# Performance work log

Measured on AMD Instinct MI355X. Metric: run time of the kernel, lower is better.

The kernel has to match this reference:

```python
import jax, jax.numpy as jnp
import numpy as np
import math

# Model dims
B, S, D, H = 2, 2048, 1024, 16
DH = D // H  # 64
TAU = 0.2
EPS = 1e-5

# Unit-scaling scale factors (constraint = gmean of fwd/bwd scales)
# Linear: gmean(fan_in**-0.5, fan_out**-0.5) = (fan_in*fan_out)**-0.25
# Matmul (m,k)@(k,n): gmean(k**-0.5, n**-0.5, m**-0.5) = (m*k*n)**(-1/6)
# Softmax over dim n: gmean(n/1.31, n/1.65) (empirical constants from unit_scaling)
# GELU: gmean(1/0.588, 1/0.675)
MM_SCALE = (S * S * DH) ** (-1.0 / 6.0)
SM_SCALE = S / math.sqrt(1.31 * 1.65)
GELU_SCALE = (0.588 * 0.675) ** -0.5
SQRT_TAU = math.sqrt(TAU)
SQRT_1MTAU = math.sqrt(1.0 - TAU)


def u_linear(x, w, b=None):
    fan_out, fan_in = w.shape
    scale = (fan_in * fan_out) ** -0.25
    y = x @ w.T
    if b is not None:
        y = y + b
    return y * scale


def layer_norm(x, w, b):
    m = jnp.mean(x, axis=-1, keepdims=True)
    v = jnp.mean(jnp.square(x - m), axis=-1, keepdims=True)
    return (x - m) * jax.lax.rsqrt(v + EPS) * w + b


def setup_inputs() -> dict:
    key = jax.random.key(0)
    ks = jax.random.split(key, 8)
    return {
        "x": jax.random.normal(ks[0], (B, S, D), jnp.float32),
        "w_qkv": jax.random.normal(ks[1], (3 * D, D), jnp.float32),
        "w_o": jax.random.normal(ks[2], (D, D), jnp.float32),
        "w1": jax.random.normal(ks[3], (4 * D, D), jnp.float32),
        "b1": jnp.zeros((4 * D,), jnp.float32),
        "w2": jax.random.normal(ks[4], (D, 4 * D), jnp.float32),
        "b2": jnp.zeros((D,), jnp.float32),
        "ln1_w": jnp.ones((D,), jnp.float32),
        "ln1_b": jnp.zeros((D,), jnp.float32),
        "ln2_w": jnp.ones((D,), jnp.float32),
        "ln2_b": jnp.zeros((D,), jnp.float32),
    }


def reference(x, w_qkv, w_o, w1, b1, w2, b2, ln1_w, ln1_b, ln2_w, ln2_b):
    # --- MHSA branch (residual_split forward is identity; tau enters at add) ---
    skip = x
    h = layer_norm(x, ln1_w, ln1_b)
    qkv = u_linear(h, w_qkv)  # [B,S,3D]
    # einops 'b s (d z h) -> z b h s d' with z=3, h=H
    qkv = qkv.reshape(B, S, DH, 3, H)
    q = jnp.transpose(qkv[:, :, :, 0, :], (0, 3, 1, 2))  # [B,H,S,DH]
    k = jnp.transpose(qkv[:, :, :, 1, :], (0, 3, 1, 2))
    v = jnp.transpose(qkv[:, :, :, 2, :], (0, 3, 1, 2))
    scores = jnp.einsum("bhsd,bhtd->bhst", q, k) * MM_SCALE
    attn = jax.nn.softmax(scores, axis=-1) * SM_SCALE
    # dropout: eval mode -> identity
    av = jnp.einsum("bhst,bhtd->bhsd", attn, v) * MM_SCALE
    av = jnp.transpose(av, (0, 2, 1, 3)).reshape(B, S, D)  # b h s d -> b s (h d)
    attn_out = u_linear(av, w_o)
    x = SQRT_TAU * attn_out + SQRT_1MTAU * skip  # residual_add

    # --- MLP branch ---
    skip = x
    h = layer_norm(x, ln2_w, ln2_b)
    h = u_linear(h, w1, b1)
    h = jax.nn.gelu(h, approximate=False) * GELU_SCALE
    h = u_linear(h, w2, b2)
    return SQRT_TAU * h + SQRT_1MTAU * skip
```

## Files before the change

kernel.cpp:

```cpp
#include <hip/hip_runtime.h>
#include <hip/hip_bf16.h>
#include <math.h>

typedef __hip_bfloat16 bf16;
typedef __attribute__((ext_vector_type(8))) short short8;
typedef __attribute__((ext_vector_type(4))) float floatx4;

#define B_   2
#define S_   2048
#define D_   1024
#define H_   16
#define DH_  64
#define BS_  4096
#define D3_  3072
#define DF_  4096

__device__ __forceinline__ float tof(float v) { return v; }
__device__ __forceinline__ float tof(bf16 v) { return __bfloat162float(v); }

__device__ __forceinline__ void gload_lds16(const bf16* g, bf16* l) {
  __builtin_amdgcn_global_load_lds(
      (const __attribute__((address_space(1))) unsigned int*)g,
      (__attribute__((address_space(3))) unsigned int*)l, 16, 0, 0);
}

#define VMCNT(n) asm volatile("s_waitcnt vmcnt(" #n ")" ::: "memory")

__global__ __launch_bounds__(256) void cvt_f32_bf16(
    const float* __restrict__ in, bf16* __restrict__ out, int n4) {
  int i = blockIdx.x * 256 + threadIdx.x;
  if (i >= n4) return;
  float4 v = ((const float4*)in)[i];
  bf16 o[4] = {__float2bfloat16(v.x), __float2bfloat16(v.y),
               __float2bfloat16(v.z), __float2bfloat16(v.w)};
  ((ulong1*)out)[i] = *(ulong1*)o;
}

__global__ __launch_bounds__(256) void cvt_all(
    const float* __restrict__ wqkv, const float* __restrict__ wo,
    const float* __restrict__ w1, bf16* __restrict__ wqb,
    bf16* __restrict__ wob, bf16* __restrict__ w1b) {
  const int g = blockIdx.x * 256 + threadIdx.x;
  if (g < 786432) {
    const int n2 = g >> 8;
    const int col = (g & 255) * 4;
    const int z = n2 >> 10, hh = (n2 >> 6) & 15, d = n2 & 63;
    const int n = d * 48 + z * 16 + hh;
    float4 v = *(const float4*)(wqkv + (size_t)n * 1024 + col);
    bf16 o[4] = {__float2bfloat16(v.x), __float2bfloat16(v.y),
                 __float2bfloat16(v.z), __float2bfloat16(v.w)};
    *(unsigned long long*)(wqb + (size_t)n2 * 1024 + col) =
        *(unsigned long long*)o;
  } else if (g < 1048576) {
    const int g2 = g - 786432;
    float4 v = ((const float4*)wo)[g2];
    bf16 o[4] = {__float2bfloat16(v.x), __float2bfloat16(v.y),
                 __float2bfloat16(v.z), __float2bfloat16(v.w)};
    ((unsigned long long*)wob)[g2] = *(unsigned long long*)o;
  } else {
    const int g2 = g - 1048576;
    float4 v = ((const float4*)w1)[g2];
    bf16 o[4] = {__float2bfloat16(v.x), __float2bfloat16(v.y),
                 __float2bfloat16(v.z), __float2bfloat16(v.w)};
    ((unsigned long long*)w1b)[g2] = *(unsigned long long*)o;
  }
}

template <bool FUSE, bool INIT, typename TA, typename TS>
__global__ __launch_bounds__(256) void resid_ln_kernel(
    const TA* __restrict__ a, const TA* __restrict__ a2,
    const TS* __restrict__ skip,
    const float* __restrict__ w, const float* __restrict__ bias,
    bf16* __restrict__ hout, float st, float s1t,
    float* __restrict__ oinit, const float* __restrict__ b2,
    float cb, float cs) {
  const int row = blockIdx.x;
  const int tid = threadIdx.x;
  const int base = tid * 4;
  const size_t roff = (size_t)row * D_;

  float xv[4];
#pragma unroll
  for (int i = 0; i < 4; i++) {
    float v = tof(a[roff + base + i]);
    if (FUSE) v = st * (v + tof(a2[roff + base + i]))
                  + s1t * tof(skip[roff + base + i]);
    xv[i] = v;
  }
  if (INIT) {
#pragma unroll
    for (int i = 0; i < 4; i++)
      oinit[roff + base + i] = cs * xv[i] + cb * b2[base + i];
  }

  float ls = 0.f, lq = 0.f;
#pragma unroll
  for (int i = 0; i < 4; i++) { ls += xv[i]; lq += xv[i] * xv[i]; }

  __shared__ float ssum[256];
  __shared__ float ssq[256];
  ssum[tid] = ls; ssq[tid] = lq;
  __syncthreads();
  for (int off = 128; off > 0; off >>= 1) {
    if (tid < off) { ssum[tid] += ssum[tid + off]; ssq[tid] += ssq[tid + off]; }
    __syncthreads();
  }
  const float mean = ssum[0] * (1.0f / D_);
  const float var  = ssq[0] * (1.0f / D_) - mean * mean;
  const float rstd = rsqrtf(var + 1e-5f);

#pragma unroll
  for (int i = 0; i < 4; i++) {
    float v = (xv[i] - mean) * rstd * w[base + i] + bias[base + i];
    hout[roff + base + i] = __float2bfloat16(v);
  }
}

__global__ __launch_bounds__(256) void reduce_ffn2(
    const bf16* __restrict__ p0, const bf16* __restrict__ p1,
    float* __restrict__ out, float sc) {
  const size_t i = ((size_t)blockIdx.x * 256 + threadIdx.x) * 8;
  short8 a = *(const short8*)(p0 + i);
  short8 b = *(const short8*)(p1 + i);
  bf16 t0[8], t1[8];
  *(short8*)t0 = a; *(short8*)t1 = b;
  float4 o0 = *(float4*)(out + i);
  float4 o1 = *(float4*)(out + i + 4);
#pragma unroll
  for (int e = 0; e < 4; e++) {
    ((float*)&o0)[e] += sc * (__bfloat162float(t0[e]) + __bfloat162float(t1[e]));
    ((float*)&o1)[e] += sc * (__bfloat162float(t0[e + 4]) + __bfloat162float(t1[e + 4]));
  }
  *(float4*)(out + i) = o0;
  *(float4*)(out + i + 4) = o1;
}

__global__ __launch_bounds__(256) void combine_attn(
    const bf16* __restrict__ O0, const bf16* __restrict__ O1,
    const float* __restrict__ l0, const float* __restrict__ l1,
    bf16* __restrict__ att, float sc) {
  const size_t i = ((size_t)blockIdx.x * 256 + threadIdx.x) * 8;
  const int srow = (int)(i >> 10);
  const int h = (int)(i >> 6) & 15;
  const float inv = sc / (l0[srow * H_ + h] + l1[srow * H_ + h]);
  short8 a = *(const short8*)(O0 + i);
  short8 b = *(const short8*)(O1 + i);
  bf16 t0[8], t1[8], o[8];
  *(short8*)t0 = a; *(short8*)t1 = b;
#pragma unroll
  for (int e = 0; e < 8; e++)
    o[e] = __float2bfloat16((tof(t0[e]) + tof(t1[e])) * inv);
  *(short8*)(att + i) = *(short8*)o;
}

template <int EPI, typename TC>
__global__ __launch_bounds__(512, 2) void gemm_mfma256(
    const bf16* __restrict__ A, const bf16* __restrict__ Bw,
    TC* __restrict__ C, int M, int N, int K, float scale,
    const float* __restrict__ bias, float st) {
  __shared__ __align__(16) bf16 As[2][2][128][64];
  __shared__ __align__(16) bf16 Bs[2][2][128][64];

  const int tid = threadIdx.x;
  const int lane = tid & 63;
  const int w = tid >> 6;
  const int wm = w >> 2;
  const int wn = w & 3;
  const int quad = lane >> 4;
  const int l16 = lane & 15;

  const int nbx = N >> 8;
  const int nwg = nbx * (M >> 8);
  int bid = blockIdx.x;
  bid = (bid & 7) * (nwg >> 3) + (bid >> 3);
  const size_t bm = (size_t)(bid / nbx) * 256;
  const size_t bn = (size_t)(bid % nbx) * 256;

  const bf16* gsrc[4][2];
  bf16* ldsp[4][2];
#pragma unroll
  for (int i = 0; i < 2; i++) {
    const int G = tid + i * 512;
    const int cr = G >> 3;
    const int gs8 = ((G & 7) ^ (cr & 7)) * 8;
    const int ra = ((cr >> 6) << 7) + (cr & 63);
    const int rb = ((cr >> 5) << 6) + (cr & 31);
    gsrc[0][i] = A  + (bm + ra) * (size_t)K + gs8;
    gsrc[2][i] = A  + (bm + ra + 64) * (size_t)K + gs8;
    gsrc[1][i] = Bw + (bn + rb) * (size_t)K + gs8;
    gsrc[3][i] = Bw + (bn + rb + 32) * (size_t)K + gs8;
    ldsp[0][i] = &As[0][0][0][0] + G * 8;
    ldsp[2][i] = &As[0][1][0][0] + G * 8;
    ldsp[1][i] = &Bs[0][0][0][0] + G * 8;
    ldsp[3][i] = &Bs[0][1][0][0] + G * 8;
  }

  auto STAGE = [&](int c, int tn) {
    const int boff = (tn & 1) * 16384;
    gload_lds16(gsrc[c][0] + (size_t)tn * 64, ldsp[c][0] + boff);
    gload_lds16(gsrc[c][1] + (size_t)tn * 64, ldsp[c][1] + boff);
  };

  const int ksw0 = (quad ^ (l16 & 7)) * 8;
  const int ksw1 = ((4 + quad) ^ (l16 & 7)) * 8;

  floatx4 acc[8][4];
#pragma unroll
  for (int i = 0; i < 8; i++)
#pragma unroll
    for (int j = 0; j < 4; j++) acc[i][j] = {0.f, 0.f, 0.f, 0.f};

  short8 af[4][2], bv[2][2];

  auto READ_A = [&](int b, int h) {
#pragma unroll
    for (int mf = 0; mf < 4; mf++) {
      const bf16* p = &As[b][h][wm * 64 + mf * 16 + l16][0];
      af[mf][0] = *(const short8*)(p + ksw0);
      af[mf][1] = *(const short8*)(p + ksw1);
    }
  };
  auto READ_B = [&](int b, int bh) {
#pragma unroll
    for (int nf = 0; nf < 2; nf++) {
      const bf16* p = &Bs[b][bh][wn * 32 + nf * 16 + l16][0];
      bv[nf][0] = *(const short8*)(p + ksw0);
      bv[nf][1] = *(const short8*)(p + ksw1);
    }
  };
  auto MFMA16 = [&](int mb, int nb) {
#pragma unroll
    for (int mf = 0; mf < 4; mf++)
#pragma unroll
      for (int nf = 0; nf < 2; nf++) {
        floatx4 c = acc[mb + mf][nb + nf];
        c = __builtin_amdgcn_mfma_f32_16x16x32_bf16(af[mf][0], bv[nf][0], c, 0, 0, 0);
        c = __builtin_amdgcn_mfma_f32_16x16x32_bf16(af[mf][1], bv[nf][1], c, 0, 0, 0);
        acc[mb + mf][nb + nf] = c;
      }
  };

  STAGE(0, 0); STAGE(1, 0); STAGE(2, 0); STAGE(3, 0);
  VMCNT(4);
  __builtin_amdgcn_s_barrier();
  __builtin_amdgcn_sched_barrier(0);

  const int NT = K >> 6;
#pragma unroll 1
  for (int t = 0; t < NT; t++) {
    const int b = t & 1;
    const bool nl = (t + 1 < NT);
    READ_A(b, 0);
    READ_B(b, 0);
    if (nl) STAGE(0, t + 1);
    __builtin_amdgcn_s_barrier();
    __builtin_amdgcn_sched_barrier(0);
    __builtin_amdgcn_s_setprio(1);
    MFMA16(0, 0);
    __builtin_amdgcn_s_setprio(0);
    if (nl) { VMCNT(2); } else { VMCNT(0); }
    __builtin_amdgcn_s_barrier();
    __builtin_amdgcn_sched_barrier(0);
    READ_B(b, 1);
    if (nl) STAGE(1, t + 1);
    __builtin_amdgcn_s_barrier();
    __builtin_amdgcn_sched_barrier(0);
    __builtin_amdgcn_s_setprio(1);
    MFMA16(0, 2);
    __builtin_amdgcn_s_setprio(0);
    __builtin_amdgcn_s_barrier();
    __builtin_amdgcn_sched_barrier(0);
    READ_A(b, 1);
    if (nl) STAGE(2, t + 1);
    __builtin_amdgcn_s_barrier();
    __builtin_amdgcn_sched_barrier(0);
    __builtin_amdgcn_s_setprio(1);
    MFMA16(4, 2);
    __builtin_amdgcn_s_setprio(0);
    __builtin_amdgcn_s_barrier();
    __builtin_amdgcn_sched_barrier(0);
    READ_B(b, 0);
    if (nl) STAGE(3, t + 1);
    __builtin_amdgcn_s_barrier();
    __builtin_amdgcn_sched_barrier(0);
    __builtin_amdgcn_s_setprio(1);
    MFMA16(4, 0);
    __builtin_amdgcn_s_setprio(0);
    if (nl) { VMCNT(4); } else { VMCNT(0); }
    __builtin_amdgcn_s_barrier();
    __builtin_amdgcn_sched_barrier(0);
  }

  float sc_eff = scale;
  if (EPI == 2) sc_eff = (bn < 1024) ? st : scale;
  float bias4[4];
  if (EPI == 1) {
#pragma unroll
    for (int j = 0; j < 4; j++) bias4[j] = bias[bn + wn * 64 + j * 16 + l16];
  }
#pragma unroll
  for (int mi = 0; mi < 8; mi++) {
    const size_t r0 = bm + wm * 128 + (mi >> 2) * 64 + (mi & 3) * 16 + quad * 4;
#pragma unroll
    for (int r = 0; r < 4; r++) {
      const size_t rowoff = (r0 + r) * (size_t)N + bn + wn * 64 + l16;
#pragma unroll
      for (int j = 0; j < 4; j++) {
        float v = acc[mi][j][r];
        if (EPI == 2) {
          ((bf16*)C)[rowoff + j * 16] = __float2bfloat16(v * sc_eff);
        } else {
          float u = (v + bias4[j]) * scale;
          float tt = u * (0.7978845608f + 0.0356774081f * u * u);
          float e = __builtin_amdgcn_exp2f(tt * 2.8853900818f);
          float th = 1.0f - 2.0f * __builtin_amdgcn_rcpf(e + 1.0f);
          ((bf16*)C)[rowoff + j * 16] =
              __float2bfloat16(0.5f * u * (1.0f + th) * st);
        }
      }
    }
  }
}

__global__ __launch_bounds__(512, 2) void gemm_mfma128(
    const bf16* __restrict__ A, const bf16* __restrict__ Bw,
    bf16* __restrict__ C, bf16* __restrict__ C2, int M, int N, int K) {
  __shared__ __align__(16) bf16 As[2][2][128][64];
  __shared__ __align__(16) bf16 Bs[2][2][64][64];

  const int tid = threadIdx.x;
  const int lane = tid & 63;
  const int w = tid >> 6;
  const int wm = w >> 2;
  const int wn = w & 3;
  const int quad = lane >> 4;
  const int l16 = lane & 15;

  const int nbx = N >> 7;
  const int nwg = nbx * (M >> 8) * 2;
  int bid = blockIdx.x;
  bid = (bid & 7) * (nwg >> 3) + (bid >> 3);
  const int split = bid & 1;
  const int tile = bid >> 1;
  const size_t bm = (size_t)(tile / nbx) * 256;
  const size_t bn = (size_t)(tile % nbx) * 128;
  const int lda = K * 2;
  const int koff = split * K;

  const bf16* gA[2][2];
  bf16* lA[2][2];
#pragma unroll
  for (int i = 0; i < 2; i++) {
    const int G = tid + i * 512;
    const int cr = G >> 3;
    const int gs8 = ((G & 7) ^ (cr & 7)) * 8;
    const int ra = ((cr >> 6) << 7) + (cr & 63);
    gA[0][i] = A + (bm + ra) * (size_t)lda + koff + gs8;
    gA[1][i] = A + (bm + ra + 64) * (size_t)lda + koff + gs8;
    lA[0][i] = &As[0][0][0][0] + G * 8;
    lA[1][i] = &As[0][1][0][0] + G * 8;
  }
  const bf16* gB[2];
  bf16* lB[2];
  {
    const int cr = tid >> 3;
    const int gs8 = ((tid & 7) ^ (cr & 7)) * 8;
    gB[0] = Bw + (bn + cr) * (size_t)lda + koff + gs8;
    gB[1] = Bw + (bn + 64 + cr) * (size_t)lda + koff + gs8;
    lB[0] = &Bs[0][0][0][0] + tid * 8;
    lB[1] = &Bs[0][1][0][0] + tid * 8;
  }

  auto STAGE_A = [&](int h, int tn) {
    const int boff = (tn & 1) * 16384;
    gload_lds16(gA[h][0] + (size_t)tn * 64, lA[h][0] + boff);
    gload_lds16(gA[h][1] + (size_t)tn * 64, lA[h][1] + boff);
  };
  auto STAGE_B = [&](int bh, int tn) {
    const int boff = (tn & 1) * 8192;
    gload_lds16(gB[bh] + (size_t)tn * 64, lB[bh] + boff);
  };

  const int ksw0 = (quad ^ (l16 & 7)) * 8;
  const int ksw1 = ((4 + quad) ^ (l16 & 7)) * 8;

  floatx4 acc[8][2];
#pragma unroll
  for (int i = 0; i < 8; i++)
#pragma unroll
    for (int j = 0; j < 2; j++) acc[i][j] = {0.f, 0.f, 0.f, 0.f};

  short8 af[4][2], bv[2][2];

  auto READ_A = [&](int b, int h) {
#pragma unroll
    for (int mf = 0; mf < 4; mf++) {
      const bf16* p = &As[b][h][wm * 64 + mf * 16 + l16][0];
      af[mf][0] = *(const short8*)(p + ksw0);
      af[mf][1] = *(const short8*)(p + ksw1);
    }
  };
  auto READ_BNF = [&](int b, int nf) {
    const bf16* p = &Bs[b][wn >> 1][(wn & 1) * 32 + nf * 16 + l16][0];
    bv[nf][0] = *(const short8*)(p + ksw0);
    bv[nf][1] = *(const short8*)(p + ksw1);
  };
  auto MFMA8 = [&](int mb, int nf) {
#pragma unroll
    for (int mf = 0; mf < 4; mf++) {
      floatx4 c = acc[mb + mf][nf];
      c = __builtin_amdgcn_mfma_f32_16x16x32_bf16(af[mf][0], bv[nf][0], c, 0, 0, 0);
      c = __builtin_amdgcn_mfma_f32_16x16x32_bf16(af[mf][1], bv[nf][1], c, 0, 0, 0);
      acc[mb + mf][nf] = c;
    }
  };

  STAGE_A(0, 0); STAGE_B(0, 0); STAGE_B(1, 0); STAGE_A(1, 0);
  VMCNT(2);
  __builtin_amdgcn_s_barrier();
  __builtin_amdgcn_sched_barrier(0);

  const int NT = K >> 6;
#pragma unroll 1
  for (int t = 0; t < NT; t++) {
    const int b = t & 1;
    const bool nl = (t + 1 < NT);
    READ_A(b, 0);
    READ_BNF(b, 0);
    if (nl) STAGE_A(0, t + 1);
    __builtin_amdgcn_s_barrier();
    __builtin_amdgcn_sched_barrier(0);
    __builtin_amdgcn_s_setprio(1);
    MFMA8(0, 0);
    __builtin_amdgcn_s_setprio(0);
    __builtin_amdgcn_s_barrier();
    __builtin_amdgcn_sched_barrier(0);
    READ_BNF(b, 1);
    if (nl) STAGE_B(0, t + 1);
    __builtin_amdgcn_s_barrier();
    __builtin_amdgcn_sched_barrier(0);
    __builtin_amdgcn_s_setprio(1);
    MFMA8(0, 1);
    __builtin_amdgcn_s_setprio(0);
    if (nl) { VMCNT(3); } else { VMCNT(0); }
    __builtin_amdgcn_s_barrier();
    __builtin_amdgcn_sched_barrier(0);
    READ_A(b, 1);
    if (nl) STAGE_B(1, t + 1);
    __builtin_amdgcn_s_barrier();
    __builtin_amdgcn_sched_barrier(0);
    __builtin_amdgcn_s_setprio(1);
    MFMA8(4, 1);
    __builtin_amdgcn_s_setprio(0);
    __builtin_amdgcn_s_barrier();
    __builtin_amdgcn_sched_barrier(0);
    if (nl) STAGE_A(1, t + 1);
    __builtin_amdgcn_s_barrier();
    __builtin_amdgcn_sched_barrier(0);
    __builtin_amdgcn_s_setprio(1);
    MFMA8(4, 0);
    __builtin_amdgcn_s_setprio(0);
    if (nl) { VMCNT(2); } else { VMCNT(0); }
    __builtin_amdgcn_s_barrier();
    __builtin_amdgcn_sched_barrier(0);
  }

  bf16* dst = split ? C2 : C;
#pragma unroll
  for (int mi = 0; mi < 8; mi++) {
    const size_t r0 = bm + wm * 128 + (mi >> 2) * 64 + (mi & 3) * 16 + quad * 4;
#pragma unroll
    for (int r = 0; r < 4; r++) {
      const size_t rowoff = (r0 + r) * (size_t)N + bn + wn * 32 + l16;
#pragma unroll
      for (int j = 0; j < 2; j++)
        dst[rowoff + j * 16] = __float2bfloat16(acc[mi][j][r]);
    }
  }
}

__global__ __launch_bounds__(512) void flash_attn_mfma(
    const bf16* __restrict__ qkv, bf16* __restrict__ O0,
    bf16* __restrict__ O1, float* __restrict__ lb0,
    float* __restrict__ lb1) {
  const int flat = (blockIdx.z * H_ + blockIdx.y) * 32 + blockIdx.x;
  const int g8 = flat & 7, slot = flat >> 3;
  const int hf = g8 * 4 + (slot >> 5);
  const int rem = slot & 31;
  const int qb = (rem >> 1) * 128;
  const int half = rem & 1;
  const int h = hf & 15, b = hf >> 4;

  const int tid = threadIdx.x;
  const int lane = tid & 63;
  const int wv = tid >> 6;
  const int quad = lane >> 4;
  const int l16 = lane & 15;

  __shared__ __align__(16) bf16 Ks[64][64];
  __shared__ __align__(16) bf16 Vt[2][64][64];
  __shared__ __align__(16) bf16 Ps[128][64];

  const bf16* Qb_ = qkv + (size_t)b * S_ * D3_ + h * DH_;
  const bf16* Kb_ = Qb_ + 1024 + (size_t)half * 1024 * D3_;
  const bf16* Vb_ = Qb_ + 2048 + (size_t)half * 1024 * D3_;

  short8 bq0, bq1;
  {
    const bf16* qrow = Qb_ + (size_t)(qb + wv * 16 + l16) * D3_ + quad * 8;
    bq0 = *(const short8*)(qrow);
    bq1 = *(const short8*)(qrow + 32);
  }

  float l_part = 0.f;
  floatx4 o[4];
#pragma unroll
  for (int fd = 0; fd < 4; fd++) o[fd] = {0.f, 0.f, 0.f, 0.f};

  const int prow = wv * 16 + l16;
  const int psw = (prow & 7) << 4;
  char* pbase = (char*)&Ps[0][0] + prow * 128;

  const bf16* ksrc =
      Kb_ + (size_t)(tid >> 3) * D3_ + (((tid & 7) ^ ((tid >> 3) & 7)) * 8);
  bf16* kdst = &Ks[0][0] + tid * 8;
  const int vj = tid & 63, vd = (tid >> 6) * 8;
  const int vjg = vj >> 3, vjr = vj & 7;

  const int ksw0 = (quad ^ (l16 & 7)) * 8;
  const int ksw1 = ((4 + quad) ^ (l16 & 7)) * 8;

  gload_lds16(ksrc, kdst);
  uint4 vreg = *(const uint4*)(Vb_ + (size_t)vj * D3_ + vd);

  const int NT = 1024 / 64;
#pragma unroll 1
  for (int t = 0; t < NT; t++) {
    const int cur = t & 1;
    {
      bf16 tmp[8];
      *(uint4*)tmp = vreg;
#pragma unroll
      for (int e = 0; e < 8; e++)
        Vt[cur][vd + e][((vjg ^ e) << 3) | vjr] = tmp[e];
    }
    __syncthreads();

    float st[4][4];
    __builtin_amdgcn_s_setprio(1);
#pragma unroll
    for (int fk = 0; fk < 4; fk++) {
      const bf16* kp = &Ks[fk * 16 + l16][0];
      short8 ak0 = *(const short8*)(kp + ksw0);
      short8 ak1 = *(const short8*)(kp + ksw1);
      floatx4 acc = {0.f, 0.f, 0.f, 0.f};
      acc = __builtin_amdgcn_mfma_f32_16x16x32_bf16(ak0, bq0, acc, 0, 0, 0);
      acc = __builtin_amdgcn_mfma_f32_16x16x32_bf16(ak1, bq1, acc, 0, 0, 0);
#pragma unroll
      for (int r = 0; r < 4; r++) st[fk][r] = acc[r];
    }
    __builtin_amdgcn_s_setprio(0);
    __syncthreads();

    if (t + 1 < NT) {
      gload_lds16(ksrc + (size_t)(t + 1) * 64 * D3_, kdst);
      vreg = *(const uint4*)(Vb_ + (size_t)((t + 1) * 64 + vj) * D3_ + vd);
    }

#pragma unroll
    for (int fk = 0; fk < 2; fk++) {
      bf16 pk[4];
#pragma unroll
      for (int r = 0; r < 4; r++) {
        const float p = __builtin_amdgcn_exp2f(st[fk][r]);
        l_part += p;
        pk[r] = __float2bfloat16(p);
      }
      *(uint2*)(pbase + ((fk * 32 + quad * 8) ^ psw)) = *(uint2*)pk;
    }
    short8 ap0 = *(const short8*)(pbase + ((quad * 16) ^ psw));
#pragma unroll
    for (int fk = 2; fk < 4; fk++) {
      bf16 pk[4];
#pragma unroll
      for (int r = 0; r < 4; r++) {
        const float p = __builtin_amdgcn_exp2f(st[fk][r]);
        l_part += p;
        pk[r] = __float2bfloat16(p);
      }
      *(uint2*)(pbase + ((fk * 32 + quad * 8) ^ psw)) = *(uint2*)pk;
    }
    short8 ap1 = *(const short8*)(pbase + ((64 + quad * 16) ^ psw));

    __builtin_amdgcn_s_setprio(1);
#pragma unroll
    for (int fd = 0; fd < 4; fd++) {
      const bf16* vp = &Vt[cur][fd * 16 + l16][0];
      short8 bv0 = *(const short8*)(vp + ksw0);
      short8 bv1 = *(const short8*)(vp + ksw1);
      o[fd] = __builtin_amdgcn_mfma_f32_16x16x32_bf16(ap0, bv0, o[fd], 0, 0, 0);
      o[fd] = __builtin_amdgcn_mfma_f32_16x16x32_bf16(ap1, bv1, o[fd], 0, 0, 0);
    }
    __builtin_amdgcn_s_setprio(0);
  }

  l_part += __shfl_xor(l_part, 16);
  l_part += __shfl_xor(l_part, 32);

  bf16* Oo = half ? O1 : O0;
  float* lo = half ? lb1 : lb0;
  if (quad == 0)
    lo[(size_t)(b * S_ + qb + wv * 16 + l16) * H_ + h] = l_part;
#pragma unroll
  for (int r = 0; r < 4; r++) {
    const size_t base =
        ((size_t)(b * S_ + qb + wv * 16 + quad * 4 + r)) * D_ + h * DH_;
#pragma unroll
    for (int fd = 0; fd < 4; fd++)
      Oo[base + fd * 16 + l16] = __float2bfloat16(o[fd][r]);
  }
}

extern "C" void kernel_launch(void* const* d_in, const int* in_sizes, int n_in,
                              void* d_out, int out_size, void* d_ws, size_t ws_size,
                              hipStream_t stream) {
  const float* x     = (const float*)d_in[0];
  const float* w_qkv = (const float*)d_in[1];
  const float* w_o   = (const float*)d_in[2];
  const float* w1    = (const float*)d_in[3];
  const float* b1    = (const float*)d_in[4];
  const float* w2    = (const float*)d_in[5];
  const float* b2    = (const float*)d_in[6];
  const float* ln1w  = (const float*)d_in[7];
  const float* ln1b  = (const float*)d_in[8];
  const float* ln2w  = (const float*)d_in[9];
  const float* ln2b  = (const float*)d_in[10];
  float* out = (float*)d_out;
  bf16* ws  = (bf16*)d_ws;

  bf16* h1   = ws;
  bf16* wqb  = ws + 4194304;
  bf16* wob  = ws + 7340032;
  bf16* qkv  = ws + 8388608;
  bf16* w1b  = ws + 25165824;
  bf16* Ob0  = ws + 20971520;
  bf16* Ob1  = ws;
  float* l0f = (float*)(ws + 4194304);
  float* l1f = l0f + 65536;
  bf16* att  = Ob0;
  bf16* w2b  = ws;
  bf16* Po   = ws + 8388608;
  bf16* h2   = ws + 4194304;
  bf16* g    = ws + 8388608;
  bf16* Pf0  = ws + 4194304;
  bf16* Pf1  = ws + 25165824;

  const float MM_SCALE   = (float)pow((double)S_ * S_ * DH_, -1.0 / 6.0);
  const float SM_SCALE   = (float)((double)S_ / sqrt(1.31 * 1.65));
  const float GELU_SCALE = (float)pow(0.588 * 0.675, -0.5);
  const float SQRT_TAU   = (float)sqrt(0.2);
  const float SQRT_1MT   = (float)sqrt(0.8);
  const float LOG2E      = 1.4426950408889634f;
  const float qkv_scale  = (float)pow((double)D_ * D3_, -0.25);
  const float o_scale    = (float)pow((double)D_ * D_, -0.25);
  const float w1_scale   = (float)pow((double)D_ * DF_, -0.25);
  const float w2_scale   = (float)pow((double)DF_ * D_, -0.25);

  cvt_all<<<8192, 256, 0, stream>>>(w_qkv, w_o, w1, wqb, wob, w1b);
  resid_ln_kernel<false, false, float, float><<<BS_, 256, 0, stream>>>(
      x, nullptr, nullptr, ln1w, ln1b, h1, 0.f, 0.f, nullptr, nullptr, 0.f, 0.f);
  gemm_mfma256<2, bf16><<<dim3(192), 512, 0, stream>>>(
      h1, wqb, qkv, BS_, D3_, D_, qkv_scale, nullptr,
      qkv_scale * MM_SCALE * LOG2E);
  flash_attn_mfma<<<dim3(32, H_, B_), 512, 0, stream>>>(
      qkv, Ob0, Ob1, l0f, l1f);
  combine_attn<<<2048, 256, 0, stream>>>(
      Ob0, Ob1, l0f, l1f, att, SM_SCALE * MM_SCALE);
  cvt_f32_bf16<<<4096, 256, 0, stream>>>(w2, w2b, D_ * DF_ / 4);
  gemm_mfma128<<<dim3(256), 512, 0, stream>>>(
      att, wob, Po, Po + (size_t)BS_ * D_, BS_, D_, D_ / 2);
  resid_ln_kernel<true, true, bf16, float><<<BS_, 256, 0, stream>>>(
      Po, Po + (size_t)BS_ * D_, x, ln2w, ln2b, h2,
      SQRT_TAU * o_scale, SQRT_1MT, out, b2, SQRT_TAU * w2_scale, SQRT_1MT);
  gemm_mfma256<1, bf16><<<dim3(256), 512, 0, stream>>>(
      h2, w1b, g, BS_, DF_, D_, w1_scale, b1, GELU_SCALE);
  gemm_mfma128<<<dim3(256), 512, 0, stream>>>(
      g, w2b, Pf0, Pf1, BS_, D_, DF_ / 2);
  reduce_ffn2<<<2048, 256, 0, stream>>>(Pf0, Pf1, out, SQRT_TAU * w2_scale);
}
```

Before: 338.4 us.

## Fuse w2 conversion into QKV GEMM grid and double-buffer K tiles in attention

Removes the separate fp32-to-bf16 conversion launch for w2 by adding 64 extra workgroups to the QKV GEMM grid that perform the conversion alongside the GEMM tiles. The flash attention kernel now double-buffers K in LDS, issuing the next tile's load before the QK^T compute and removing one __syncthreads per iteration. Workspace buffers are remapped, with attention partials placed in the output buffer and the GEMM outputs split into low and high halves. This lets everything fit, at the cost of extra LDS in attention and more complex addressing.

```diff
diff --git a/kernel.cpp b/kernel.cpp
--- a/kernel.cpp
+++ b/kernel.cpp
@@ -25,16 +25,6 @@
 }
 
 #define VMCNT(n) asm volatile("s_waitcnt vmcnt(" #n ")" ::: "memory")
-
-__global__ __launch_bounds__(256) void cvt_f32_bf16(
-    const float* __restrict__ in, bf16* __restrict__ out, int n4) {
-  int i = blockIdx.x * 256 + threadIdx.x;
-  if (i >= n4) return;
-  float4 v = ((const float4*)in)[i];
-  bf16 o[4] = {__float2bfloat16(v.x), __float2bfloat16(v.y),
-               __float2bfloat16(v.z), __float2bfloat16(v.w)};
-  ((ulong1*)out)[i] = *(ulong1*)o;
-}
 
 __global__ __launch_bounds__(256) void cvt_all(
     const float* __restrict__ wqkv, const float* __restrict__ wo,
@@ -153,11 +143,27 @@
   *(short8*)(att + i) = *(short8*)o;
 }
 
-template <int EPI, typename TC>
+template <int EPI, bool FCVT, typename TC>
 __global__ __launch_bounds__(512, 2) void gemm_mfma256(
     const bf16* __restrict__ A, const bf16* __restrict__ Bw,
-    TC* __restrict__ C, int M, int N, int K, float scale,
-    const float* __restrict__ bias, float st) {
+    TC* __restrict__ C, TC* __restrict__ Chi,
+    int M, int N, int K, float scale,
+    const float* __restrict__ bias, float st,
+    const float* __restrict__ cvsrc, bf16* __restrict__ cvdst, int cvn4) {
+  const int nbx = N >> 8;
+  const int nwg = nbx * (M >> 8);
+  if (FCVT && (int)blockIdx.x >= nwg) {
+    const int nth = ((int)gridDim.x - nwg) * 512;
+    for (int i = ((int)blockIdx.x - nwg) * 512 + (int)threadIdx.x; i < cvn4;
+         i += nth) {
+      float4 v = ((const float4*)cvsrc)[i];
+      bf16 o[4] = {__float2bfloat16(v.x), __float2bfloat16(v.y),
+                   __float2bfloat16(v.z), __float2bfloat16(v.w)};
+      ((unsigned long long*)cvdst)[i] = *(unsigned long long*)o;
+    }
+    return;
+  }
+
   __shared__ __align__(16) bf16 As[2][2][128][64];
   __shared__ __align__(16) bf16 Bs[2][2][128][64];
 
@@ -169,8 +175,6 @@
   const int quad = lane >> 4;
   const int l16 = lane & 15;
 
-  const int nbx = N >> 8;
-  const int nwg = nbx * (M >> 8);
   int bid = blockIdx.x;
   bid = (bid & 7) * (nwg >> 3) + (bid >> 3);
   const size_t bm = (size_t)(bid / nbx) * 256;
@@ -291,6 +295,8 @@
     __builtin_amdgcn_sched_barrier(0);
   }
 
+  TC* Cb = (bm < 1024) ? C : Chi;
+  const size_t rsub = (bm < 1024) ? 0 : 1024;
   float sc_eff = scale;
   if (EPI == 2) sc_eff = (bn < 1024) ? st : scale;
   float bias4[4];
@@ -300,7 +306,8 @@
   }
 #pragma unroll
   for (int mi = 0; mi < 8; mi++) {
-    const size_t r0 = bm + wm * 128 + (mi >> 2) * 64 + (mi & 3) * 16 + quad * 4;
+    const size_t r0 =
+        bm - rsub + wm * 128 + (mi >> 2) * 64 + (mi & 3) * 16 + quad * 4;
 #pragma unroll
     for (int r = 0; r < 4; r++) {
       const size_t rowoff = (r0 + r) * (size_t)N + bn + wn * 64 + l16;
@@ -308,13 +315,13 @@
       for (int j = 0; j < 4; j++) {
         float v = acc[mi][j][r];
         if (EPI == 2) {
-          ((bf16*)C)[rowoff + j * 16] = __float2bfloat16(v * sc_eff);
+          Cb[rowoff + j * 16] = __float2bfloat16(v * sc_eff);
         } else {
           float u = (v + bias4[j]) * scale;
           float tt = u * (0.7978845608f + 0.0356774081f * u * u);
           float e = __builtin_amdgcn_exp2f(tt * 2.8853900818f);
           float th = 1.0f - 2.0f * __builtin_amdgcn_rcpf(e + 1.0f);
-          ((bf16*)C)[rowoff + j * 16] =
+          Cb[rowoff + j * 16] =
               __float2bfloat16(0.5f * u * (1.0f + th) * st);
         }
       }
@@ -323,7 +330,8 @@
 }
 
 __global__ __launch_bounds__(512, 2) void gemm_mfma128(
-    const bf16* __restrict__ A, const bf16* __restrict__ Bw,
+    const bf16* __restrict__ A, const bf16* __restrict__ Ahi,
+    const bf16* __restrict__ Bw,
     bf16* __restrict__ C, bf16* __restrict__ C2, int M, int N, int K) {
   __shared__ __align__(16) bf16 As[2][2][128][64];
   __shared__ __align__(16) bf16 Bs[2][2][64][64];
@@ -347,6 +355,9 @@
   const int lda = K * 2;
   const int koff = split * K;
 
+  const bf16* Ab = (bm < 1024) ? A : Ahi;
+  const size_t bmr = (bm < 1024) ? bm : bm - 1024;
+
   const bf16* gA[2][2];
   bf16* lA[2][2];
 #pragma unroll
@@ -355,8 +366,8 @@
     const int cr = G >> 3;
     const int gs8 = ((G & 7) ^ (cr & 7)) * 8;
     const int ra = ((cr >> 6) << 7) + (cr & 63);
-    gA[0][i] = A + (bm + ra) * (size_t)lda + koff + gs8;
-    gA[1][i] = A + (bm + ra + 64) * (size_t)lda + koff + gs8;
+    gA[0][i] = Ab + (bmr + ra) * (size_t)lda + koff + gs8;
+    gA[1][i] = Ab + (bmr + ra + 64) * (size_t)lda + koff + gs8;
     lA[0][i] = &As[0][0][0][0] + G * 8;
     lA[1][i] = &As[0][1][0][0] + G * 8;
   }
@@ -497,7 +508,7 @@
   const int quad = lane >> 4;
   const int l16 = lane & 15;
 
-  __shared__ __align__(16) bf16 Ks[64][64];
+  __shared__ __align__(16) bf16 Ks[2][64][64];
   __shared__ __align__(16) bf16 Vt[2][64][64];
   __shared__ __align__(16) bf16 Ps[128][64];
 
@@ -523,7 +534,7 @@
 
   const bf16* ksrc =
       Kb_ + (size_t)(tid >> 3) * D3_ + (((tid & 7) ^ ((tid >> 3) & 7)) * 8);
-  bf16* kdst = &Ks[0][0] + tid * 8;
+  bf16* kdst = &Ks[0][0][0] + tid * 8;
   const int vj = tid & 63, vd = (tid >> 6) * 8;
   const int vjg = vj >> 3, vjr = vj & 7;
 
@@ -546,11 +557,16 @@
     }
     __syncthreads();
 
+    if (t + 1 < NT) {
+      gload_lds16(ksrc + (size_t)(t + 1) * 64 * D3_, kdst + (cur ^ 1) * 4096);
+      vreg = *(const uint4*)(Vb_ + (size_t)((t + 1) * 64 + vj) * D3_ + vd);
+    }
+
     float st[4][4];
     __builtin_amdgcn_s_setprio(1);
 #pragma unroll
     for (int fk = 0; fk < 4; fk++) {
-      const bf16* kp = &Ks[fk * 16 + l16][0];
+      const bf16* kp = &Ks[cur][fk * 16 + l16][0];
       short8 ak0 = *(const short8*)(kp + ksw0);
       short8 ak1 = *(const short8*)(kp + ksw1);
       floatx4 acc = {0.f, 0.f, 0.f, 0.f};
@@ -560,12 +576,6 @@
       for (int r = 0; r < 4; r++) st[fk][r] = acc[r];
     }
     __builtin_amdgcn_s_setprio(0);
-    __syncthreads();
-
-    if (t + 1 < NT) {
-      gload_lds16(ksrc + (size_t)(t + 1) * 64 * D3_, kdst);
-      vreg = *(const uint4*)(Vb_ + (size_t)((t + 1) * 64 + vj) * D3_ + vd);
-    }
 
 #pragma unroll
     for (int fk = 0; fk < 2; fk++) {
@@ -642,16 +652,17 @@
   bf16* wqb  = ws + 4194304;
   bf16* wob  = ws + 7340032;
   bf16* qkv  = ws + 8388608;
+  bf16* w2b  = ws + 20971520;
   bf16* w1b  = ws + 25165824;
-  bf16* Ob0  = ws + 20971520;
-  bf16* Ob1  = ws;
+  bf16* Ob0  = (bf16*)out;
+  bf16* Ob1  = (bf16*)out + 4194304;
   float* l0f = (float*)(ws + 4194304);
   float* l1f = l0f + 65536;
-  bf16* att  = Ob0;
-  bf16* w2b  = ws;
+  bf16* att  = ws;
   bf16* Po   = ws + 8388608;
   bf16* h2   = ws + 4194304;
-  bf16* g    = ws + 8388608;
+  bf16* gl   = ws;
+  bf16* gh   = ws + 8388608;
   bf16* Pf0  = ws + 4194304;
   bf16* Pf1  = ws + 25165824;
 
@@ -669,22 +680,23 @@
   cvt_all<<<8192, 256, 0, stream>>>(w_qkv, w_o, w1, wqb, wob, w1b);
   resid_ln_kernel<false, false, float, float><<<BS_, 256, 0, stream>>>(
       x, nullptr, nullptr, ln1w, ln1b, h1, 0.f, 0.f, nullptr, nullptr, 0.f, 0.f);
-  gemm_mfma256<2, bf16><<<dim3(192), 512, 0, stream>>>(
-      h1, wqb, qkv, BS_, D3_, D_, qkv_scale, nullptr,
-      qkv_scale * MM_SCALE * LOG2E);
+  gemm_mfma256<2, true, bf16><<<dim3(256), 512, 0, stream>>>(
+      h1, wqb, qkv, qkv + (size_t)1024 * D3_, BS_, D3_, D_, qkv_scale,
+      nullptr, qkv_scale * MM_SCALE * LOG2E, w2, w2b, D_ * DF_ / 4);
   flash_attn_mfma<<<dim3(32, H_, B_), 512, 0, stream>>>(
       qkv, Ob0, Ob1, l0f, l1f);
   combine_attn<<<2048, 256, 0, stream>>>(
       Ob0, Ob1, l0f, l1f, att, SM_SCALE * MM_SCALE);
-  cvt_f32_bf16<<<4096, 256, 0, stream>>>(w2, w2b, D_ * DF_ / 4);
   gemm_mfma128<<<dim3(256), 512, 0, stream>>>(
-      att, wob, Po, Po + (size_t)BS_ * D_, BS_, D_, D_ / 2);
+      att, att + (size_t)1024 * D_, wob, Po, Po + (size_t)BS_ * D_,
+      BS_, D_, D_ / 2);
   resid_ln_kernel<true, true, bf16, float><<<BS_, 256, 0, stream>>>(
       Po, Po + (size_t)BS_ * D_, x, ln2w, ln2b, h2,
       SQRT_TAU * o_scale, SQRT_1MT, out, b2, SQRT_TAU * w2_scale, SQRT_1MT);
-  gemm_mfma256<1, bf16><<<dim3(256), 512, 0, stream>>>(
-      h2, w1b, g, BS_, DF_, D_, w1_scale, b1, GELU_SCALE);
+  gemm_mfma256<1, false, bf16><<<dim3(256), 512, 0, stream>>>(
+      h2, w1b, gl, gh, BS_, DF_, D_, w1_scale, b1, GELU_SCALE,
+      nullptr, nullptr, 0);
   gemm_mfma128<<<dim3(256), 512, 0, stream>>>(
-      g, w2b, Pf0, Pf1, BS_, D_, DF_ / 2);
+      gl, gh, w2b, Pf0, Pf1, BS_, D_, DF_ / 2);
   reduce_ffn2<<<2048, 256, 0, stream>>>(Pf0, Pf1, out, SQRT_TAU * w2_scale);
 }
```

New measurement: 332.3 us. No clear change (-1.8%).
